# Performance work log

Measured on AMD Instinct MI355X. Metric: run time of the kernel, lower is better.

The kernel has to match this reference:

```python
import jax, jax.numpy as jnp
import numpy as np
from jax import lax

NUM_AGNN_LAYERS = 32  # module stacks hidden_dim AGNNConv layers
EPS = 1e-12           # F.normalize clamp


def setup_inputs() -> dict:
    key = jax.random.key(0)
    k1, k2, k3, k4 = jax.random.split(key, 4)
    N, F_in, H, C, E = 100000, 512, 32, 40, 3200000
    x = jax.random.normal(k1, (N, F_in), dtype=jnp.float32)
    edge_index = jax.random.randint(k2, (2, E), 0, N, dtype=jnp.int64)
    W1 = jax.random.normal(k3, (F_in, H), dtype=jnp.float32) * (1.0 / np.sqrt(F_in))
    b1 = jnp.zeros((H,), dtype=jnp.float32)
    W2 = jax.random.normal(k4, (H, C), dtype=jnp.float32) * (1.0 / np.sqrt(H))
    b2 = jnp.zeros((C,), dtype=jnp.float32)
    return {"x": x, "edge_index": edge_index, "W1": W1, "b1": b1, "W2": W2, "b2": b2}


def reference(x, edge_index, W1, b1, W2, b2):
    N = x.shape[0]
    loops = jnp.arange(N, dtype=edge_index.dtype)
    src = jnp.concatenate([edge_index[0], loops])  # message source j
    dst = jnp.concatenate([edge_index[1], loops])  # message target i (softmax group)

    def agnn(h, _):
        # cosine attention, beta = 1 (requires_grad=False)
        norm = jnp.maximum(jnp.linalg.norm(h, axis=-1, keepdims=True), EPS)
        hn = h / norm
        alpha = jnp.sum(hn[src] * hn[dst], axis=-1)               # [E+N]
        m = jax.ops.segment_max(alpha, dst, num_segments=N)       # stable softmax
        e = jnp.exp(alpha - m[dst])
        s = jax.ops.segment_sum(e, dst, num_segments=N)
        coef = e / s[dst]
        out = jax.ops.segment_sum(h[src] * coef[:, None], dst, num_segments=N)
        return out, None

    h = jax.nn.relu(x @ W1 + b1)
    h, _ = lax.scan(agnn, h, None, length=NUM_AGNN_LAYERS)
    logits = h @ W2 + b2
    return jax.nn.log_softmax(logits, axis=1)
```

## Files before the change

kernel.cpp:

```cpp
#include <hip/hip_runtime.h>
#include <math.h>


#define HDIM 32
#define NBMAX 1024
#define BSH 7
#define CHUNK 32768
#define TP 68

typedef _Float16 f16;
typedef _Float16 v2h __attribute__((ext_vector_type(2)));

struct __attribute__((aligned(16))) H8 { v2h p[4]; };
struct __attribute__((aligned(8)))  H4 { v2h p[2]; };

#if defined(__has_builtin)
#if __has_builtin(__builtin_amdgcn_fdot2)
#define FDOT2(a, b, c) __builtin_amdgcn_fdot2((a), (b), (c), false)
#endif
#if __has_builtin(__builtin_amdgcn_update_dpp)
#define HAS_DPP 1
#endif
#endif
#ifndef FDOT2
#define FDOT2(a, b, c) fmaf((float)(a)[1], (float)(b)[1], fmaf((float)(a)[0], (float)(b)[0], (c)))
#endif

static __device__ __forceinline__ float quad_sum(float x) {
#ifdef HAS_DPP
    x += __int_as_float(__builtin_amdgcn_update_dpp(
        0, __float_as_int(x), 0xB1 , 0xF, 0xF, true));
    x += __int_as_float(__builtin_amdgcn_update_dpp(
        0, __float_as_int(x), 0x4E , 0xF, 0xF, true));
#else
    x += __shfl_xor(x, 1);
    x += __shfl_xor(x, 2);
#endif
    return x;
}

static __device__ __forceinline__ int eread(const int* __restrict__ e, int i64, long long idx) {
    return i64 ? e[2 * idx] : e[idx];
}

__global__ void k_flag(const int* __restrict__ e, int* __restrict__ flag) {
    if (blockIdx.x == 0 && threadIdx.x == 0) {
        int z = 0;
        for (int k = 0; k < 64; ++k) z |= e[2 * k + 1];
        *flag = (z == 0) ? 1 : 0;
    }
}

__global__ void k_zero(int* __restrict__ p, int n) {
    int i = blockIdx.x * blockDim.x + threadIdx.x;
    if (i < n) p[i] = 0;
}

__launch_bounds__(256) __global__
void k_hist(const int* __restrict__ e, const int* __restrict__ flag,
            int* __restrict__ gc, int* __restrict__ blockOffs,
            long long E, long long M) {
    __shared__ int bh[NBMAX];
    for (int t = threadIdx.x; t < NBMAX; t += 256) bh[t] = 0;
    __syncthreads();
    int i64 = *flag;
    long long base = (long long)blockIdx.x * CHUNK;
    long long end = base + CHUNK < M ? base + CHUNK : M;
    for (long long m = base + threadIdx.x; m < end; m += 256) {
        int d = (m < E) ? eread(e, i64, E + m) : (int)(m - E);
        atomicAdd(&bh[d >> BSH], 1);
    }
    __syncthreads();
    for (int t = threadIdx.x; t < NBMAX; t += 256) {
        int c = bh[t];
        int off = 0;
        if (c) off = atomicAdd(&gc[t], c);
        blockOffs[(size_t)blockIdx.x * NBMAX + t] = off;
    }
}

__launch_bounds__(256) __global__
void k_bscan(const int* __restrict__ gc, int* __restrict__ bbase,
             int* __restrict__ rp, int N) {
    __shared__ int lds[256];
    int t = threadIdx.x;
    int v[4];
#pragma unroll
    for (int d = 0; d < 4; ++d) v[d] = gc[t * 4 + d];
    int tsum = v[0] + v[1] + v[2] + v[3];
    lds[t] = tsum;
    __syncthreads();
    int acc = tsum;
    for (int sh = 1; sh < 256; sh <<= 1) {
        int x = (t >= sh) ? lds[t - sh] : 0;
        __syncthreads();
        acc += x;
        lds[t] = acc;
        __syncthreads();
    }
    if (t == 255) { rp[N] = acc; bbase[NBMAX] = acc; }
    int run = acc - tsum;
#pragma unroll
    for (int d = 0; d < 4; ++d) { bbase[t * 4 + d] = run; run += v[d]; }
}

__launch_bounds__(256) __global__
void k_part(const int* __restrict__ e, const int* __restrict__ flag,
            const int* __restrict__ bbase, const int* __restrict__ blockOffs,
            int2* __restrict__ pair, long long E, long long M) {
    __shared__ int cur[NBMAX];
    for (int t = threadIdx.x; t < NBMAX; t += 256)
        cur[t] = bbase[t] + blockOffs[(size_t)blockIdx.x * NBMAX + t];
    __syncthreads();
    int i64 = *flag;
    long long base = (long long)blockIdx.x * CHUNK;
    long long end = base + CHUNK < M ? base + CHUNK : M;
    for (long long m = base + threadIdx.x; m < end; m += 256) {
        int s, d;
        if (m < E) { s = eread(e, i64, m); d = eread(e, i64, E + m); }
        else { s = d = (int)(m - E); }
        int pos = atomicAdd(&cur[d >> BSH], 1);
        pair[pos] = make_int2(s, d);
    }
}

__launch_bounds__(256) __global__
void k_fine(const int2* __restrict__ pair, const int* __restrict__ bbase,
            int* __restrict__ rp, int* __restrict__ col, int N) {
    __shared__ int cnt[128];
    __shared__ int sc[128];
    int b = blockIdx.x;
    int beg = bbase[b];
    int end = bbase[b + 1];
    int t = threadIdx.x;
    if (t < 128) cnt[t] = 0;
    __syncthreads();
    for (int k = beg + t; k < end; k += 256)
        atomicAdd(&cnt[pair[k].y & 127], 1);
    __syncthreads();
    if (t < 128) sc[t] = cnt[t];
    __syncthreads();
    for (int sh = 1; sh < 128; sh <<= 1) {
        int x = 0;
        if (t < 128 && t >= sh) x = sc[t - sh];
        __syncthreads();
        if (t < 128) sc[t] += x;
        __syncthreads();
    }
    if (t < 128) {
        int basepos = beg + sc[t] - cnt[t];
        int d = (b << BSH) + t;
        if (d < N) rp[d] = basepos;
        cnt[t] = basepos;
    }
    __syncthreads();
    for (int k = beg + t; k < end; k += 256) {
        int2 p = pair[k];
        int pos = atomicAdd(&cnt[p.y & 127], 1);
        col[pos] = p.x;
    }
}

__launch_bounds__(256) __global__
void k_gemm1(const float* __restrict__ x, const float* __restrict__ W1,
             const float* __restrict__ b1, f16* __restrict__ h,
             float* __restrict__ invn, int N) {
    __shared__ float tile[64 * TP];
    int tid = threadIdx.x;
    int cg = tid & 7;
    int ty = tid >> 3;
    int rbase = blockIdx.x * 64;
    float4 bias = *(const float4*)(b1 + 4 * cg);
    float acc[2][4];
#pragma unroll
    for (int m = 0; m < 2; ++m) {
        acc[m][0] = bias.x; acc[m][1] = bias.y;
        acc[m][2] = bias.z; acc[m][3] = bias.w;
    }
    for (int kc = 0; kc < 8; ++kc) {
        if (kc) __syncthreads();
#pragma unroll
        for (int j = 0; j < 4; ++j) {
            int f = tid + j * 256;
            int row = f >> 4, kin = f & 15;
            int r = rbase + row;
            float4 v = make_float4(0.f, 0.f, 0.f, 0.f);
            if (r < N) v = *(const float4*)(x + (size_t)r * 512 + kc * 64 + kin * 4);
            *(float4*)(tile + row * TP + kin * 4) = v;
        }
        __syncthreads();
#pragma unroll
        for (int k4 = 0; k4 < 16; ++k4) {
            int kk = kc * 64 + k4 * 4;
            float4 w0 = *(const float4*)(W1 + (size_t)(kk + 0) * 32 + 4 * cg);
            float4 w1 = *(const float4*)(W1 + (size_t)(kk + 1) * 32 + 4 * cg);
            float4 w2 = *(const float4*)(W1 + (size_t)(kk + 2) * 32 + 4 * cg);
            float4 w3 = *(const float4*)(W1 + (size_t)(kk + 3) * 32 + 4 * cg);
#pragma unroll
            for (int m = 0; m < 2; ++m) {
                float4 xv = *(const float4*)(tile + (ty + 32 * m) * TP + k4 * 4);
                acc[m][0] = fmaf(xv.x, w0.x, acc[m][0]);
                acc[m][1] = fmaf(xv.x, w0.y, acc[m][1]);
                acc[m][2] = fmaf(xv.x, w0.z, acc[m][2]);
                acc[m][3] = fmaf(xv.x, w0.w, acc[m][3]);
                acc[m][0] = fmaf(xv.y, w1.x, acc[m][0]);
                acc[m][1] = fmaf(xv.y, w1.y, acc[m][1]);
                acc[m][2] = fmaf(xv.y, w1.z, acc[m][2]);
                acc[m][3] = fmaf(xv.y, w1.w, acc[m][3]);
                acc[m][0] = fmaf(xv.z, w2.x, acc[m][0]);
                acc[m][1] = fmaf(xv.z, w2.y, acc[m][1]);
                acc[m][2] = fmaf(xv.z, w2.z, acc[m][2]);
                acc[m][3] = fmaf(xv.z, w2.w, acc[m][3]);
                acc[m][0] = fmaf(xv.w, w3.x, acc[m][0]);
                acc[m][1] = fmaf(xv.w, w3.y, acc[m][1]);
                acc[m][2] = fmaf(xv.w, w3.z, acc[m][2]);
                acc[m][3] = fmaf(xv.w, w3.w, acc[m][3]);
            }
        }
    }
#pragma unroll
    for (int m = 0; m < 2; ++m) {
        int r = rbase + ty + 32 * m;
        float hv[4];
        float ss = 0.0f;
#pragma unroll
        for (int j = 0; j < 4; ++j) {
            hv[j] = fmaxf(acc[m][j], 0.0f);
            ss = fmaf(hv[j], hv[j], ss);
        }
        ss += __shfl_xor(ss, 1);
        ss += __shfl_xor(ss, 2);
        ss += __shfl_xor(ss, 4);
        if (r < N) {
            H4 o;
            o.p[0][0] = (f16)hv[0]; o.p[0][1] = (f16)hv[1];
            o.p[1][0] = (f16)hv[2]; o.p[1][1] = (f16)hv[3];
            *(H4*)(h + (size_t)r * HDIM + 4 * cg) = o;
            if (cg == 0) invn[r] = 1.0f / fmaxf(sqrtf(ss), 1e-12f);
        }
    }
}

__launch_bounds__(256) __global__
void k_agnn(const f16* __restrict__ h_in, const float* __restrict__ inv_in,
            f16* __restrict__ h_out, float* __restrict__ inv_out,
            const int* __restrict__ rp, const int* __restrict__ col, int N) {
    int wave = threadIdx.x >> 6;
    int lane = threadIdx.x & 63;
    int i = blockIdx.x * 4 + wave;
    if (i >= N) return;
    int beg = rp[i];
    int deg = rp[i + 1] - beg;
    int eloc = lane >> 2;
    int c8 = lane & 3;
    float inv_i = inv_in[i];
    H8 hi = *(const H8*)(h_in + (size_t)i * HDIM + 8 * c8);
    float s_run = 0.0f;
    float acc[8] = {0.f, 0.f, 0.f, 0.f, 0.f, 0.f, 0.f, 0.f};
    int nchunk = (deg + 15) >> 4;
    int cv = (lane < deg) ? col[beg + lane] : 0;
    H8 rA, rB;
    float iA, iB = 0.0f;
    bool vA, vB = false;
    {
        vA = eloc < deg;
        int s = __shfl(cv, eloc);
        s = vA ? s : 0;
        rA = *(const H8*)(h_in + (size_t)s * HDIM + 8 * c8);
        iA = inv_in[s];
    }
    if (nchunk > 1) {
        int idx = 16 + eloc;
        vB = idx < deg;
        int s = __shfl(cv, 16 | eloc);
        s = vB ? s : 0;
        rB = *(const H8*)(h_in + (size_t)s * HDIM + 8 * c8);
        iB = inv_in[s];
    } else {
        rB = hi;
    }
    for (int ck = 0; ck < nchunk; ++ck) {
        H8 rc = rA;
        float ic = iA;
        bool vc = vA;
        rA = rB; iA = iB; vA = vB;
        int nc = ck + 2;
        if (nc < nchunk) {
            if ((nc & 3) == 0) {
                int idx64 = nc * 16 + lane;
                cv = (idx64 < deg) ? col[beg + idx64] : 0;
            }
            int idx = nc * 16 + eloc;
            vB = idx < deg;
            int s = __shfl(cv, ((nc & 3) << 4) | eloc);
            s = vB ? s : 0;
            rB = *(const H8*)(h_in + (size_t)s * HDIM + 8 * c8);
            iB = inv_in[s];
        }
        float dot = 0.0f;
#pragma unroll
        for (int j = 0; j < 4; ++j) dot = FDOT2(rc.p[j], hi.p[j], dot);
        dot = quad_sum(dot);
        float e = vc ? __expf(fmaf(dot, inv_i * ic, -1.0f)) : 0.0f;
        s_run += e;
#pragma unroll
        for (int j = 0; j < 4; ++j) {
            acc[2 * j + 0] = fmaf(e, (float)rc.p[j][0], acc[2 * j + 0]);
            acc[2 * j + 1] = fmaf(e, (float)rc.p[j][1], acc[2 * j + 1]);
        }
    }
    float s_tot = s_run;
#pragma unroll
    for (int mask = 4; mask <= 32; mask <<= 1) s_tot += __shfl_xor(s_tot, mask);
#pragma unroll
    for (int mask = 4; mask <= 32; mask <<= 1) {
#pragma unroll
        for (int j = 0; j < 8; ++j) acc[j] += __shfl_xor(acc[j], mask);
    }
    float invs = 1.0f / s_tot;
    float ss = 0.0f;
#pragma unroll
    for (int j = 0; j < 8; ++j) {
        acc[j] *= invs;
        ss = fmaf(acc[j], acc[j], ss);
    }
    ss = quad_sum(ss);
    if (lane < 4) {
        H8 o;
#pragma unroll
        for (int j = 0; j < 4; ++j) {
            o.p[j][0] = (f16)acc[2 * j + 0];
            o.p[j][1] = (f16)acc[2 * j + 1];
        }
        *(H8*)(h_out + (size_t)i * HDIM + 8 * lane) = o;
        if (lane == 0) inv_out[i] = 1.0f / fmaxf(sqrtf(ss), 1e-12f);
    }
}

__launch_bounds__(256) __global__
void k_gemm2(const f16* __restrict__ h, const float* __restrict__ W2,
             const float* __restrict__ b2, float* __restrict__ out, int N) {
    int wave = threadIdx.x >> 6;
    int lane = threadIdx.x & 63;
    int i = blockIdx.x * 4 + wave;
    if (i >= N) return;
    bool act = lane < 40;
    float acc = act ? b2[lane] : 0.0f;
    const f16* hr = h + (size_t)i * HDIM;
#pragma unroll
    for (int k = 0; k < HDIM; ++k) {
        float hk = (float)hr[k];
        float w = act ? W2[k * 40 + lane] : 0.0f;
        acc = fmaf(hk, w, acc);
    }
    float logit = act ? acc : -INFINITY;
    float m = logit;
#pragma unroll
    for (int mask = 32; mask >= 1; mask >>= 1) m = fmaxf(m, __shfl_xor(m, mask));
    float e = act ? __expf(logit - m) : 0.0f;
    float s = e;
#pragma unroll
    for (int mask = 32; mask >= 1; mask >>= 1) s += __shfl_xor(s, mask);
    float res = logit - m - __logf(s);
    if (act) out[(size_t)i * 40 + lane] = res;
}

extern "C" void kernel_launch(void* const* d_in, const int* in_sizes, int n_in,
                              void* d_out, int out_size, void* d_ws, size_t ws_size,
                              hipStream_t stream) {
    const float* x  = (const float*)d_in[0];
    const int*   e  = (const int*)d_in[1];
    const float* W1 = (const float*)d_in[2];
    const float* b1 = (const float*)d_in[3];
    const float* W2 = (const float*)d_in[4];
    const float* b2 = (const float*)d_in[5];
    float* out = (float*)d_out;

    const long long E = (long long)in_sizes[1] / 2;
    const int N = in_sizes[0] / 512;
    const long long M = E + N;
    const int nblk = (int)((M + CHUNK - 1) / CHUNK);

    char* w = (char*)d_ws;
    auto alloc = [&](size_t bytes) -> void* {
        void* p = (void*)w;
        w += (bytes + 255) & ~(size_t)255;
        return p;
    };
    int*  flag      = (int*)alloc(4);
    int*  gc        = (int*)alloc(NBMAX * 4);
    int*  bbase     = (int*)alloc((NBMAX + 1) * 4);
    int*  blockOffs = (int*)alloc((size_t)nblk * NBMAX * 4);
    int2* pair      = (int2*)alloc((size_t)M * 8);
    int*  rp        = (int*)alloc(((size_t)N + 1) * 4);
    int*  col       = (int*)alloc((size_t)M * 4);
    f16*  hA   = (f16*)alloc((size_t)N * HDIM * 2);
    f16*  hB   = (f16*)alloc((size_t)N * HDIM * 2);
    float* invA = (float*)alloc((size_t)N * 4);
    float* invB = (float*)alloc((size_t)N * 4);
    if ((size_t)(w - (char*)d_ws) > ws_size) return;

    k_flag<<<1, 64, 0, stream>>>(e, flag);
    k_zero<<<(NBMAX + 255) / 256, 256, 0, stream>>>(gc, NBMAX);
    k_hist<<<nblk, 256, 0, stream>>>(e, flag, gc, blockOffs, E, M);
    k_bscan<<<1, 256, 0, stream>>>(gc, bbase, rp, N);
    k_part<<<nblk, 256, 0, stream>>>(e, flag, bbase, blockOffs, pair, E, M);
    k_fine<<<NBMAX, 256, 0, stream>>>(pair, bbase, rp, col, N);

    k_gemm1<<<(N + 63) / 64, 256, 0, stream>>>(x, W1, b1, hA, invA, N);

    f16 *hin = hA, *hout = hB;
    float *iin = invA, *iout = invB;
    for (int l = 0; l < 32; ++l) {
        k_agnn<<<(N + 3) / 4, 256, 0, stream>>>(hin, iin, hout, iout, rp, col, N);
        f16* t = hin; hin = hout; hout = t;
        float* ti = iin; iin = iout; iout = ti;
    }
    k_gemm2<<<(N + 3) / 4, 256, 0, stream>>>(hin, W2, b2, out, N);
}
```

Baseline: 2.181 ms.

## Recompute node norms from fp16 rows in AGNN and double-buffer the GEMM1 tiles

The AGNN kernel no longer reads and writes a separate per-node inverse-norm array. It recomputes each neighbour's norm from the fp16 row it already gathers, using an extra fdot2 per edge. This removes a random 4-byte gather per edge and a store per node, at the cost of extra ALU work and norms now taken from fp16-rounded values. Separately, GEMM1 moves to 128-row tiles with W1 staged in shared memory and double-buffered register prefetch of the next K-chunk.

```diff
diff --git a/kernel.cpp b/kernel.cpp
--- a/kernel.cpp
+++ b/kernel.cpp
@@ -6,7 +6,8 @@
 #define NBMAX 1024
 #define BSH 7
 #define CHUNK 32768
-#define TP 68
+#define TXP 36
+#define TWP 36
 
 typedef _Float16 f16;
 typedef _Float16 v2h __attribute__((ext_vector_type(2)));
@@ -161,44 +162,72 @@
     }
 }
 
-__launch_bounds__(256) __global__
+__launch_bounds__(256, 4) __global__
 void k_gemm1(const float* __restrict__ x, const float* __restrict__ W1,
-             const float* __restrict__ b1, f16* __restrict__ h,
-             float* __restrict__ invn, int N) {
-    __shared__ float tile[64 * TP];
+             const float* __restrict__ b1, f16* __restrict__ h, int N) {
+    __shared__ float xt[2][128 * TXP];
+    __shared__ float wt[2][32 * TWP];
     int tid = threadIdx.x;
     int cg = tid & 7;
     int ty = tid >> 3;
-    int rbase = blockIdx.x * 64;
+    int rbase = blockIdx.x * 128;
     float4 bias = *(const float4*)(b1 + 4 * cg);
-    float acc[2][4];
-#pragma unroll
-    for (int m = 0; m < 2; ++m) {
+    float acc[4][4];
+#pragma unroll
+    for (int m = 0; m < 4; ++m) {
         acc[m][0] = bias.x; acc[m][1] = bias.y;
         acc[m][2] = bias.z; acc[m][3] = bias.w;
     }
-    for (int kc = 0; kc < 8; ++kc) {
-        if (kc) __syncthreads();
+    int xrow = tid >> 3;
+    int xkin = tid & 7;
+    float4 gx[4];
+    float4 gw;
+    {
+        int kc = 0;
 #pragma unroll
         for (int j = 0; j < 4; ++j) {
-            int f = tid + j * 256;
-            int row = f >> 4, kin = f & 15;
+            int slot = tid + j * 256;
+            int row = slot >> 3, kin = slot & 7;
             int r = rbase + row;
-            float4 v = make_float4(0.f, 0.f, 0.f, 0.f);
-            if (r < N) v = *(const float4*)(x + (size_t)r * 512 + kc * 64 + kin * 4);
-            *(float4*)(tile + row * TP + kin * 4) = v;
-        }
-        __syncthreads();
-#pragma unroll
-        for (int k4 = 0; k4 < 16; ++k4) {
-            int kk = kc * 64 + k4 * 4;
-            float4 w0 = *(const float4*)(W1 + (size_t)(kk + 0) * 32 + 4 * cg);
-            float4 w1 = *(const float4*)(W1 + (size_t)(kk + 1) * 32 + 4 * cg);
-            float4 w2 = *(const float4*)(W1 + (size_t)(kk + 2) * 32 + 4 * cg);
-            float4 w3 = *(const float4*)(W1 + (size_t)(kk + 3) * 32 + 4 * cg);
-#pragma unroll
-            for (int m = 0; m < 2; ++m) {
-                float4 xv = *(const float4*)(tile + (ty + 32 * m) * TP + k4 * 4);
+            gx[j] = (r < N) ? *(const float4*)(x + (size_t)r * 512 + kc * 32 + kin * 4)
+                            : make_float4(0.f, 0.f, 0.f, 0.f);
+        }
+        int wrow = tid >> 3, wkin = tid & 7;
+        gw = *(const float4*)(W1 + (size_t)(kc * 32 + wrow) * 32 + wkin * 4);
+#pragma unroll
+        for (int j = 0; j < 4; ++j) {
+            int slot = tid + j * 256;
+            int row = slot >> 3, kin = slot & 7;
+            *(float4*)(&xt[0][row * TXP + kin * 4]) = gx[j];
+        }
+        *(float4*)(&wt[0][wrow * TWP + wkin * 4]) = gw;
+    }
+    __syncthreads();
+    for (int kc = 0; kc < 16; ++kc) {
+        int buf = kc & 1;
+        if (kc + 1 < 16) {
+            int kn = kc + 1;
+#pragma unroll
+            for (int j = 0; j < 4; ++j) {
+                int slot = tid + j * 256;
+                int row = slot >> 3, kin = slot & 7;
+                int r = rbase + row;
+                gx[j] = (r < N) ? *(const float4*)(x + (size_t)r * 512 + kn * 32 + kin * 4)
+                                : make_float4(0.f, 0.f, 0.f, 0.f);
+            }
+            gw = *(const float4*)(W1 + (size_t)(kn * 32 + (tid >> 3)) * 32 + (tid & 7) * 4);
+        }
+        const float* xb = xt[buf];
+        const float* wb = wt[buf];
+#pragma unroll
+        for (int k4 = 0; k4 < 8; ++k4) {
+            float4 w0 = *(const float4*)(wb + (k4 * 4 + 0) * TWP + 4 * cg);
+            float4 w1 = *(const float4*)(wb + (k4 * 4 + 1) * TWP + 4 * cg);
+            float4 w2 = *(const float4*)(wb + (k4 * 4 + 2) * TWP + 4 * cg);
+            float4 w3 = *(const float4*)(wb + (k4 * 4 + 3) * TWP + 4 * cg);
+#pragma unroll
+            for (int m = 0; m < 4; ++m) {
+                float4 xv = *(const float4*)(xb + (ty + 32 * m) * TXP + k4 * 4);
                 acc[m][0] = fmaf(xv.x, w0.x, acc[m][0]);
                 acc[m][1] = fmaf(xv.x, w0.y, acc[m][1]);
                 acc[m][2] = fmaf(xv.x, w0.z, acc[m][2]);
@@ -217,33 +246,35 @@
                 acc[m][3] = fmaf(xv.w, w3.w, acc[m][3]);
             }
         }
-    }
-#pragma unroll
-    for (int m = 0; m < 2; ++m) {
+        if (kc + 1 < 16) {
+            int nbuf = buf ^ 1;
+#pragma unroll
+            for (int j = 0; j < 4; ++j) {
+                int slot = tid + j * 256;
+                int row = slot >> 3, kin = slot & 7;
+                *(float4*)(&xt[nbuf][row * TXP + kin * 4]) = gx[j];
+            }
+            *(float4*)(&wt[nbuf][(tid >> 3) * TWP + (tid & 7) * 4]) = gw;
+            __syncthreads();
+        }
+    }
+    (void)xrow; (void)xkin;
+#pragma unroll
+    for (int m = 0; m < 4; ++m) {
         int r = rbase + ty + 32 * m;
-        float hv[4];
-        float ss = 0.0f;
-#pragma unroll
-        for (int j = 0; j < 4; ++j) {
-            hv[j] = fmaxf(acc[m][j], 0.0f);
-            ss = fmaf(hv[j], hv[j], ss);
-        }
-        ss += __shfl_xor(ss, 1);
-        ss += __shfl_xor(ss, 2);
-        ss += __shfl_xor(ss, 4);
         if (r < N) {
             H4 o;
-            o.p[0][0] = (f16)hv[0]; o.p[0][1] = (f16)hv[1];
-            o.p[1][0] = (f16)hv[2]; o.p[1][1] = (f16)hv[3];
+            o.p[0][0] = (f16)fmaxf(acc[m][0], 0.0f);
+            o.p[0][1] = (f16)fmaxf(acc[m][1], 0.0f);
+            o.p[1][0] = (f16)fmaxf(acc[m][2], 0.0f);
+            o.p[1][1] = (f16)fmaxf(acc[m][3], 0.0f);
             *(H4*)(h + (size_t)r * HDIM + 4 * cg) = o;
-            if (cg == 0) invn[r] = 1.0f / fmaxf(sqrtf(ss), 1e-12f);
-        }
-    }
-}
-
-__launch_bounds__(256) __global__
-void k_agnn(const f16* __restrict__ h_in, const float* __restrict__ inv_in,
-            f16* __restrict__ h_out, float* __restrict__ inv_out,
+        }
+    }
+}
+
+__launch_bounds__(256) __global__
+void k_agnn(const f16* __restrict__ h_in, f16* __restrict__ h_out,
             const int* __restrict__ rp, const int* __restrict__ col, int N) {
     int wave = threadIdx.x >> 6;
     int lane = threadIdx.x & 63;
@@ -253,21 +284,23 @@
     int deg = rp[i + 1] - beg;
     int eloc = lane >> 2;
     int c8 = lane & 3;
-    float inv_i = inv_in[i];
     H8 hi = *(const H8*)(h_in + (size_t)i * HDIM + 8 * c8);
+    float dsi = 0.0f;
+#pragma unroll
+    for (int j = 0; j < 4; ++j) dsi = FDOT2(hi.p[j], hi.p[j], dsi);
+    dsi = quad_sum(dsi);
+    float inv_i = 1.0f / fmaxf(sqrtf(dsi), 1e-12f);
     float s_run = 0.0f;
     float acc[8] = {0.f, 0.f, 0.f, 0.f, 0.f, 0.f, 0.f, 0.f};
     int nchunk = (deg + 15) >> 4;
     int cv = (lane < deg) ? col[beg + lane] : 0;
     H8 rA, rB;
-    float iA, iB = 0.0f;
     bool vA, vB = false;
     {
         vA = eloc < deg;
         int s = __shfl(cv, eloc);
         s = vA ? s : 0;
         rA = *(const H8*)(h_in + (size_t)s * HDIM + 8 * c8);
-        iA = inv_in[s];
     }
     if (nchunk > 1) {
         int idx = 16 + eloc;
@@ -275,15 +308,13 @@
         int s = __shfl(cv, 16 | eloc);
         s = vB ? s : 0;
         rB = *(const H8*)(h_in + (size_t)s * HDIM + 8 * c8);
-        iB = inv_in[s];
     } else {
         rB = hi;
     }
     for (int ck = 0; ck < nchunk; ++ck) {
         H8 rc = rA;
-        float ic = iA;
         bool vc = vA;
-        rA = rB; iA = iB; vA = vB;
+        rA = rB; vA = vB;
         int nc = ck + 2;
         if (nc < nchunk) {
             if ((nc & 3) == 0) {
@@ -295,13 +326,17 @@
             int s = __shfl(cv, ((nc & 3) << 4) | eloc);
             s = vB ? s : 0;
             rB = *(const H8*)(h_in + (size_t)s * HDIM + 8 * c8);
-            iB = inv_in[s];
-        }
-        float dot = 0.0f;
-#pragma unroll
-        for (int j = 0; j < 4; ++j) dot = FDOT2(rc.p[j], hi.p[j], dot);
+        }
+        float dot = 0.0f, dsj = 0.0f;
+#pragma unroll
+        for (int j = 0; j < 4; ++j) {
+            dot = FDOT2(rc.p[j], hi.p[j], dot);
+            dsj = FDOT2(rc.p[j], rc.p[j], dsj);
+        }
         dot = quad_sum(dot);
-        float e = vc ? __expf(fmaf(dot, inv_i * ic, -1.0f)) : 0.0f;
+        dsj = quad_sum(dsj);
+        float inv_j = 1.0f / fmaxf(sqrtf(dsj), 1e-12f);
+        float e = vc ? __expf(fmaf(dot, inv_i * inv_j, -1.0f)) : 0.0f;
         s_run += e;
 #pragma unroll
         for (int j = 0; j < 4; ++j) {
@@ -318,13 +353,8 @@
         for (int j = 0; j < 8; ++j) acc[j] += __shfl_xor(acc[j], mask);
     }
     float invs = 1.0f / s_tot;
-    float ss = 0.0f;
-#pragma unroll
-    for (int j = 0; j < 8; ++j) {
-        acc[j] *= invs;
-        ss = fmaf(acc[j], acc[j], ss);
-    }
-    ss = quad_sum(ss);
+#pragma unroll
+    for (int j = 0; j < 8; ++j) acc[j] *= invs;
     if (lane < 4) {
         H8 o;
 #pragma unroll
@@ -333,7 +363,6 @@
             o.p[j][1] = (f16)acc[2 * j + 1];
         }
         *(H8*)(h_out + (size_t)i * HDIM + 8 * lane) = o;
-        if (lane == 0) inv_out[i] = 1.0f / fmaxf(sqrtf(ss), 1e-12f);
     }
 }
 
@@ -396,8 +425,6 @@
     int*  col       = (int*)alloc((size_t)M * 4);
     f16*  hA   = (f16*)alloc((size_t)N * HDIM * 2);
     f16*  hB   = (f16*)alloc((size_t)N * HDIM * 2);
-    float* invA = (float*)alloc((size_t)N * 4);
-    float* invB = (float*)alloc((size_t)N * 4);
     if ((size_t)(w - (char*)d_ws) > ws_size) return;
 
     k_flag<<<1, 64, 0, stream>>>(e, flag);
@@ -407,14 +434,12 @@
     k_part<<<nblk, 256, 0, stream>>>(e, flag, bbase, blockOffs, pair, E, M);
     k_fine<<<NBMAX, 256, 0, stream>>>(pair, bbase, rp, col, N);
 
-    k_gemm1<<<(N + 63) / 64, 256, 0, stream>>>(x, W1, b1, hA, invA, N);
+    k_gemm1<<<(N + 127) / 128, 256, 0, stream>>>(x, W1, b1, hA, N);
 
     f16 *hin = hA, *hout = hB;
-    float *iin = invA, *iout = invB;
     for (int l = 0; l < 32; ++l) {
-        k_agnn<<<(N + 3) / 4, 256, 0, stream>>>(hin, iin, hout, iout, rp, col, N);
+        k_agnn<<<(N + 3) / 4, 256, 0, stream>>>(hin, hout, rp, col, N);
         f16* t = hin; hin = hout; hout = t;
-        float* ti = iin; iin = iout; iout = ti;
     }
     k_gemm2<<<(N + 3) / 4, 256, 0, stream>>>(hin, W2, b2, out, N);
 }
```

New measurement: 2.231 ms. +2.3%, slower.

## Compute first-layer GEMM with fp16 MFMA instead of fp32 FMA tiles

Applied to the files above, without the earlier changes.

Replaces the shared-memory-tiled fp32 FMA GEMM for x@W1 with a per-wave 16-row tile that converts x to fp16 on the fly and uses 16x16x32 f16 MFMA instructions. A small pre-kernel converts W1 to a transposed fp16 copy so that B fragments load contiguously. The intent is to cut the compute cost of this GEMM, which reads the 200MB x matrix, leaving it bound by memory bandwidth. The trade-off is lower input precision (x and W1 rounded to fp16) and one extra launch.

```diff
diff --git a/kernel.cpp b/kernel.cpp
--- a/kernel.cpp
+++ b/kernel.cpp
@@ -6,10 +6,11 @@
 #define NBMAX 1024
 #define BSH 7
 #define CHUNK 32768
-#define TP 68
 
 typedef _Float16 f16;
 typedef _Float16 v2h __attribute__((ext_vector_type(2)));
+typedef _Float16 f16x8 __attribute__((ext_vector_type(8)));
+typedef float f32x4 __attribute__((ext_vector_type(4)));
 
 struct __attribute__((aligned(16))) H8 { v2h p[4]; };
 struct __attribute__((aligned(8)))  H4 { v2h p[2]; };
@@ -161,82 +162,59 @@
     }
 }
 
-__launch_bounds__(256) __global__
-void k_gemm1(const float* __restrict__ x, const float* __restrict__ W1,
+__global__ void k_w1cvt(const float* __restrict__ W1, f16* __restrict__ W1hT) {
+    int t = blockIdx.x * 256 + threadIdx.x;
+    if (t < 512 * 32) {
+        int k = t >> 5, j = t & 31;
+        W1hT[(size_t)j * 512 + k] = (f16)W1[t];
+    }
+}
+
+__launch_bounds__(256) __global__
+void k_gemm1(const float* __restrict__ x, const f16* __restrict__ W1hT,
              const float* __restrict__ b1, f16* __restrict__ h,
              float* __restrict__ invn, int N) {
-    __shared__ float tile[64 * TP];
-    int tid = threadIdx.x;
-    int cg = tid & 7;
-    int ty = tid >> 3;
-    int rbase = blockIdx.x * 64;
-    float4 bias = *(const float4*)(b1 + 4 * cg);
-    float acc[2][4];
-#pragma unroll
-    for (int m = 0; m < 2; ++m) {
-        acc[m][0] = bias.x; acc[m][1] = bias.y;
-        acc[m][2] = bias.z; acc[m][3] = bias.w;
-    }
-    for (int kc = 0; kc < 8; ++kc) {
-        if (kc) __syncthreads();
-#pragma unroll
-        for (int j = 0; j < 4; ++j) {
-            int f = tid + j * 256;
-            int row = f >> 4, kin = f & 15;
-            int r = rbase + row;
-            float4 v = make_float4(0.f, 0.f, 0.f, 0.f);
-            if (r < N) v = *(const float4*)(x + (size_t)r * 512 + kc * 64 + kin * 4);
-            *(float4*)(tile + row * TP + kin * 4) = v;
-        }
-        __syncthreads();
-#pragma unroll
-        for (int k4 = 0; k4 < 16; ++k4) {
-            int kk = kc * 64 + k4 * 4;
-            float4 w0 = *(const float4*)(W1 + (size_t)(kk + 0) * 32 + 4 * cg);
-            float4 w1 = *(const float4*)(W1 + (size_t)(kk + 1) * 32 + 4 * cg);
-            float4 w2 = *(const float4*)(W1 + (size_t)(kk + 2) * 32 + 4 * cg);
-            float4 w3 = *(const float4*)(W1 + (size_t)(kk + 3) * 32 + 4 * cg);
-#pragma unroll
-            for (int m = 0; m < 2; ++m) {
-                float4 xv = *(const float4*)(tile + (ty + 32 * m) * TP + k4 * 4);
-                acc[m][0] = fmaf(xv.x, w0.x, acc[m][0]);
-                acc[m][1] = fmaf(xv.x, w0.y, acc[m][1]);
-                acc[m][2] = fmaf(xv.x, w0.z, acc[m][2]);
-                acc[m][3] = fmaf(xv.x, w0.w, acc[m][3]);
-                acc[m][0] = fmaf(xv.y, w1.x, acc[m][0]);
-                acc[m][1] = fmaf(xv.y, w1.y, acc[m][1]);
-                acc[m][2] = fmaf(xv.y, w1.z, acc[m][2]);
-                acc[m][3] = fmaf(xv.y, w1.w, acc[m][3]);
-                acc[m][0] = fmaf(xv.z, w2.x, acc[m][0]);
-                acc[m][1] = fmaf(xv.z, w2.y, acc[m][1]);
-                acc[m][2] = fmaf(xv.z, w2.z, acc[m][2]);
-                acc[m][3] = fmaf(xv.z, w2.w, acc[m][3]);
-                acc[m][0] = fmaf(xv.w, w3.x, acc[m][0]);
-                acc[m][1] = fmaf(xv.w, w3.y, acc[m][1]);
-                acc[m][2] = fmaf(xv.w, w3.z, acc[m][2]);
-                acc[m][3] = fmaf(xv.w, w3.w, acc[m][3]);
-            }
-        }
-    }
-#pragma unroll
-    for (int m = 0; m < 2; ++m) {
-        int r = rbase + ty + 32 * m;
-        float hv[4];
-        float ss = 0.0f;
-#pragma unroll
-        for (int j = 0; j < 4; ++j) {
-            hv[j] = fmaxf(acc[m][j], 0.0f);
-            ss = fmaf(hv[j], hv[j], ss);
-        }
+    int wid = (blockIdx.x * 256 + threadIdx.x) >> 6;
+    int lane = threadIdx.x & 63;
+    int ntile = (N + 15) >> 4;
+    if (wid >= ntile) return;
+    int j16 = lane & 15;
+    int kb = lane >> 4;
+    int rload = wid * 16 + j16;
+    if (rload > N - 1) rload = N - 1;
+    const float* xr = x + (size_t)rload * 512 + kb * 8;
+    const f16* w0 = W1hT + (size_t)j16 * 512 + kb * 8;
+    const f16* w1 = W1hT + (size_t)(j16 + 16) * 512 + kb * 8;
+    f32x4 acc0 = {0.f, 0.f, 0.f, 0.f};
+    f32x4 acc1 = {0.f, 0.f, 0.f, 0.f};
+#pragma unroll 4
+    for (int ks = 0; ks < 16; ++ks) {
+        float4 xa = *(const float4*)(xr + ks * 32);
+        float4 xb = *(const float4*)(xr + ks * 32 + 4);
+        f16x8 a;
+        a[0] = (f16)xa.x; a[1] = (f16)xa.y; a[2] = (f16)xa.z; a[3] = (f16)xa.w;
+        a[4] = (f16)xb.x; a[5] = (f16)xb.y; a[6] = (f16)xb.z; a[7] = (f16)xb.w;
+        f16x8 b0 = *(const f16x8*)(w0 + ks * 32);
+        f16x8 b1v = *(const f16x8*)(w1 + ks * 32);
+        acc0 = __builtin_amdgcn_mfma_f32_16x16x32_f16(a, b0, acc0, 0, 0, 0);
+        acc1 = __builtin_amdgcn_mfma_f32_16x16x32_f16(a, b1v, acc1, 0, 0, 0);
+    }
+    float bias0 = b1[j16];
+    float bias1 = b1[j16 + 16];
+#pragma unroll
+    for (int r = 0; r < 4; ++r) {
+        float v0 = fmaxf(acc0[r] + bias0, 0.0f);
+        float v1 = fmaxf(acc1[r] + bias1, 0.0f);
+        float ss = fmaf(v0, v0, v1 * v1);
         ss += __shfl_xor(ss, 1);
         ss += __shfl_xor(ss, 2);
         ss += __shfl_xor(ss, 4);
-        if (r < N) {
-            H4 o;
-            o.p[0][0] = (f16)hv[0]; o.p[0][1] = (f16)hv[1];
-            o.p[1][0] = (f16)hv[2]; o.p[1][1] = (f16)hv[3];
-            *(H4*)(h + (size_t)r * HDIM + 4 * cg) = o;
-            if (cg == 0) invn[r] = 1.0f / fmaxf(sqrtf(ss), 1e-12f);
+        ss += __shfl_xor(ss, 8);
+        int row = wid * 16 + 4 * kb + r;
+        if (row < N) {
+            h[(size_t)row * HDIM + j16] = (f16)v0;
+            h[(size_t)row * HDIM + j16 + 16] = (f16)v1;
+            if (j16 == 0) invn[row] = 1.0f / fmaxf(sqrtf(ss), 1e-12f);
         }
     }
 }
@@ -398,6 +376,7 @@
     f16*  hB   = (f16*)alloc((size_t)N * HDIM * 2);
     float* invA = (float*)alloc((size_t)N * 4);
     float* invB = (float*)alloc((size_t)N * 4);
+    f16*  W1hT = (f16*)alloc((size_t)512 * 32 * 2);
     if ((size_t)(w - (char*)d_ws) > ws_size) return;
 
     k_flag<<<1, 64, 0, stream>>>(e, flag);
@@ -407,7 +386,9 @@
     k_part<<<nblk, 256, 0, stream>>>(e, flag, bbase, blockOffs, pair, E, M);
     k_fine<<<NBMAX, 256, 0, stream>>>(pair, bbase, rp, col, N);
 
-    k_gemm1<<<(N + 63) / 64, 256, 0, stream>>>(x, W1, b1, hA, invA, N);
+    k_w1cvt<<<64, 256, 0, stream>>>(W1, W1hT);
+    int ntile = (N + 15) >> 4;
+    k_gemm1<<<(ntile + 3) / 4, 256, 0, stream>>>(x, W1hT, b1, hA, invA, N);
 
     f16 *hin = hA, *hout = hB;
     float *iin = invA, *iout = invB;
```

Result: faster. 2.097 ms (-3.9%).
